# Optimization experiments

Hardware: AMD Instinct MI355X
Metric: run time of the kernel (lower is better)

The kernel has to match this reference:

```python
import jax, jax.numpy as jnp
import numpy as np

T_STEPS = 16
A = 64
B = 64
N = 16          # read_N
C = 3           # channels
H = 1024        # enc_size
IN = N * N * C  # LSTM input size = 768
EPS = 1e-8


def setup_inputs() -> dict:
    key = jax.random.key(0)
    ks = jax.random.split(key, 12)
    s = 0.02
    x = jax.random.normal(ks[0], (1024, C, B, A), dtype=jnp.float32)
    W_att = jax.random.normal(ks[1], (5, H), dtype=jnp.float32) * s
    b_att = jnp.zeros((5,), dtype=jnp.float32)
    W_ih = jax.random.normal(ks[2], (4 * H, IN), dtype=jnp.float32) * s
    W_hh = jax.random.normal(ks[3], (4 * H, H), dtype=jnp.float32) * s
    b_ih = jnp.zeros((4 * H,), dtype=jnp.float32)
    b_hh = jnp.zeros((4 * H,), dtype=jnp.float32)
    W_fc0 = jax.random.normal(ks[4], (H, H), dtype=jnp.float32) * s
    b_fc0 = jnp.zeros((H,), dtype=jnp.float32)
    W_fc = jax.random.normal(ks[5], (10, H), dtype=jnp.float32) * s
    b_fc = jnp.zeros((10,), dtype=jnp.float32)
    return {"x": x, "W_att": W_att, "b_att": b_att, "W_ih": W_ih, "W_hh": W_hh,
            "b_ih": b_ih, "b_hh": b_hh, "W_fc0": W_fc0, "b_fc0": b_fc0,
            "W_fc": W_fc, "b_fc": b_fc}


def _filterbank(gx, gy, sigma2, delta):
    # gx, gy, sigma2, delta: [Bt]
    grid = jnp.arange(N, dtype=jnp.float32)
    mu_x = gx[:, None] + (grid - N / 2 - 0.5) * delta[:, None]   # [Bt, N]
    mu_y = gy[:, None] + (grid - N / 2 - 0.5) * delta[:, None]   # [Bt, N]
    a = jnp.arange(A, dtype=jnp.float32)
    b = jnp.arange(B, dtype=jnp.float32)
    s2 = sigma2[:, None, None]
    Fx = jnp.exp(-(a[None, None, :] - mu_x[:, :, None]) ** 2 / (2 * s2))  # [Bt,N,A]
    Fy = jnp.exp(-(b[None, None, :] - mu_y[:, :, None]) ** 2 / (2 * s2))  # [Bt,N,B]
    Fx = Fx / (Fx.sum(2, keepdims=True) + EPS)
    Fy = Fy / (Fy.sum(2, keepdims=True) + EPS)
    return Fx, Fy


def _forward(x, W_att, b_att, W_ih, W_hh, b_ih, b_hh, W_fc0, b_fc0, W_fc, b_fc):
    Bt = x.shape[0]
    img = x.reshape(Bt, C, B, A)
    h0 = jnp.zeros((Bt, H), dtype=x.dtype)
    c0 = jnp.zeros((Bt, H), dtype=x.dtype)

    def step(carry, _):
        h, c = carry
        p = h @ W_att.T + b_att                      # [Bt, 5]
        gx_, gy_, log_s2, log_d, log_g = (p[:, 0], p[:, 1], p[:, 2], p[:, 3], p[:, 4])
        gx = (A + 1) / 2 * (gx_ + 1)
        gy = (B + 1) / 2 * (gy_ + 1)
        delta = (max(A, B) - 1) / (N - 1) * jnp.exp(log_d)
        sigma2 = jnp.exp(log_s2)
        gamma = jnp.exp(log_g)
        Fx, Fy = _filterbank(gx, gy, sigma2, delta)
        # glimpse[b,c] = Fy @ img[b,c] @ Fx^T -> [Bt, C, N, N]
        glimpse = jnp.einsum('bny,bcya,bxa->bcnx', Fy, img, Fx)
        r = glimpse.reshape(Bt, IN) * gamma[:, None]
        gates = r @ W_ih.T + b_ih + h @ W_hh.T + b_hh
        i_g, f_g, g_g, o_g = jnp.split(gates, 4, axis=1)
        c_new = jax.nn.sigmoid(f_g) * c + jax.nn.sigmoid(i_g) * jnp.tanh(g_g)
        h_new = jax.nn.sigmoid(o_g) * jnp.tanh(c_new)
        return (h_new, c_new), None

    (h, _), _ = jax.lax.scan(step, (h0, c0), None, length=T_STEPS)
    t = jax.nn.relu(h @ W_fc0.T + b_fc0)
    return t @ W_fc.T + b_fc


def reference(x, W_att, b_att, W_ih, W_hh, b_ih, b_hh, W_fc0, b_fc0, W_fc, b_fc):
    return _forward(x, W_att, b_att, W_ih, W_hh, b_ih, b_hh, W_fc0, b_fc0, W_fc, b_fc)
```

## Files before the change

### kernel.cpp

```cpp
#include <hip/hip_runtime.h>

typedef unsigned short u16;
typedef unsigned int u32;
typedef _Float16 f16;
typedef _Float16 half8 __attribute__((ext_vector_type(8)));
typedef _Float16 half4 __attribute__((ext_vector_type(4)));
typedef float f32x4 __attribute__((ext_vector_type(4)));

#define SPLIT_SC 2048.0f
#define SPLIT_INV (1.0f / 2048.0f)

__device__ __forceinline__ float sigf(float x) { return 1.0f / (1.0f + expf(-x)); }

__global__ __launch_bounds__(256) void att_glimpse(
    const f16* __restrict__ h_hi, const f16* __restrict__ h_lo,
    const float* __restrict__ Watt, const float* __restrict__ batt,
    const float* __restrict__ x,
    f16* __restrict__ r_hi, f16* __restrict__ r_lo)
{
    __shared__ float simg[64 * 64];
    __shared__ float sFx[16 * 68];
    __shared__ float sFyT[64 * 20];
    __shared__ float stmp[16 * 68];
    __shared__ float sred[4 * 5];
    __shared__ float spar[8];

    const int b = blockIdx.x, tid = threadIdx.x;
    const int lane = tid & 63, wave = tid >> 6;

    float p[5] = {0.f, 0.f, 0.f, 0.f, 0.f};
    {
        const f16* hh = h_hi + (size_t)b * 1024;
        const f16* hl = h_lo + (size_t)b * 1024;
        for (int k = tid; k < 1024; k += 256) {
            float hv = (float)hh[k] + (float)hl[k] * SPLIT_INV;
#pragma unroll
            for (int j = 0; j < 5; j++) p[j] += hv * Watt[j * 1024 + k];
        }
#pragma unroll
        for (int j = 0; j < 5; j++) {
#pragma unroll
            for (int o = 32; o > 0; o >>= 1) p[j] += __shfl_xor(p[j], o);
        }
        if (lane == 0) {
#pragma unroll
            for (int j = 0; j < 5; j++) sred[wave * 5 + j] = p[j];
        }
    }
    __syncthreads();
    if (tid == 0) {
        float q[5];
#pragma unroll
        for (int j = 0; j < 5; j++)
            q[j] = sred[j] + sred[5 + j] + sred[10 + j] + sred[15 + j] + batt[j];
        float q2 = fminf(fmaxf(q[2], -60.f), 60.f);
        float q3 = fminf(fmaxf(q[3], -60.f), 60.f);
        float q4 = fminf(fmaxf(q[4], -60.f), 60.f);
        spar[0] = 32.5f * (q[0] + 1.0f);
        spar[1] = 32.5f * (q[1] + 1.0f);
        spar[2] = 0.5f * expf(-q2);
        spar[3] = 4.2f * expf(q3);
        spar[4] = expf(q4);
    }
    __syncthreads();
    const float gx = spar[0], gy = spar[1], inv2s2 = spar[2], dl = spar[3],
                gamma = spar[4];

    {
        const float af = (float)lane;
#pragma unroll
        for (int i = 0; i < 4; i++) {
            int n = wave + i * 4;
            float nn = (float)n - 8.5f;
            float mux = gx + nn * dl;
            float ex = af - mux;
            float vx = expf(-ex * ex * inv2s2);
            float sx = vx;
#pragma unroll
            for (int o = 32; o > 0; o >>= 1) sx += __shfl_xor(sx, o);
            sFx[n * 68 + lane] = vx / (sx + 1e-8f);

            float muy = gy + nn * dl;
            float ey = af - muy;
            float vy = expf(-ey * ey * inv2s2);
            float sy = vy;
#pragma unroll
            for (int o = 32; o > 0; o >>= 1) sy += __shfl_xor(sy, o);
            sFyT[lane * 20 + n] = vy / (sy + 1e-8f);
        }
    }

    for (int c = 0; c < 3; c++) {
        __syncthreads();
        {
            const float4* src = (const float4*)(x + (size_t)b * 12288 + c * 4096);
            float4* dst = (float4*)simg;
            for (int i = tid; i < 1024; i += 256) dst[i] = src[i];
        }
        __syncthreads();

        {
            const int n4 = wave, ysub = lane >> 4, a4 = lane & 15;
            f32x4 acc[4];
#pragma unroll
            for (int j = 0; j < 4; j++) acc[j] = (f32x4)(0.f);
            for (int yy = 0; yy < 16; yy++) {
                int y = ysub * 16 + yy;
                float4 im = *(const float4*)(simg + y * 64 + a4 * 4);
                float4 fy = *(const float4*)(sFyT + y * 20 + n4 * 4);
                f32x4 iv = {im.x, im.y, im.z, im.w};
                acc[0] += fy.x * iv;
                acc[1] += fy.y * iv;
                acc[2] += fy.z * iv;
                acc[3] += fy.w * iv;
            }
#pragma unroll
            for (int j = 0; j < 4; j++) {
#pragma unroll
                for (int o = 16; o <= 32; o <<= 1) {
                    acc[j].x += __shfl_xor(acc[j].x, o);
                    acc[j].y += __shfl_xor(acc[j].y, o);
                    acc[j].z += __shfl_xor(acc[j].z, o);
                    acc[j].w += __shfl_xor(acc[j].w, o);
                }
            }
            if (ysub == 0) {
#pragma unroll
                for (int j = 0; j < 4; j++)
                    *(f32x4*)(stmp + (n4 * 4 + j) * 68 + a4 * 4) = acc[j];
            }
        }
        __syncthreads();

        {
            const int n = tid >> 4, xo = tid & 15;
            const float* tp = stmp + n * 68;
            const float* fx = sFx + xo * 68;
            float s = 0.f;
            for (int a = 0; a < 64; a += 4) {
                float4 t4 = *(const float4*)(tp + a);
                float4 x4 = *(const float4*)(fx + a);
                s += t4.x * x4.x + t4.y * x4.y + t4.z * x4.z + t4.w * x4.w;
            }
            float v = s * gamma;
            f16 hi = (f16)v;
            size_t idx = (size_t)b * 768 + c * 256 + tid;
            r_hi[idx] = hi;
            r_lo[idx] = (f16)((v - (float)hi) * SPLIT_SC);
        }
    }
}

__global__ __launch_bounds__(256) void swz_w(
    const float* __restrict__ W1, const float* __restrict__ W2,
    f16* __restrict__ out)
{
    const int kc = blockIdx.x >> 5, bn = blockIdx.x & 31;
    for (int t = threadIdx.x; t < 512; t += 256) {
        int c = t >> 6, lane = t & 63, l15 = lane & 15, lq = lane >> 4;
        int gate = ((c & 1) << 1) + (l15 >> 3);
        int ul   = ((c >> 1) << 3) + (l15 & 7);
        int wrow = gate * 1024 + bn * 32 + ul;
        const float* src;
        if (kc < 24) src = W1 + (size_t)wrow * 768 + kc * 32 + lq * 8;
        else         src = W2 + (size_t)wrow * 1024 + (kc - 24) * 32 + lq * 8;
        float4 g0 = *(const float4*)src;
        float4 g1 = *(const float4*)(src + 4);
        float gv[8] = {g0.x, g0.y, g0.z, g0.w, g1.x, g1.y, g1.z, g1.w};
        half8 hv, lv;
#pragma unroll
        for (int j = 0; j < 8; j++) {
            f16 h = (f16)gv[j];
            hv[j] = h;
            lv[j] = (f16)((gv[j] - (float)h) * SPLIT_SC);
        }
        size_t base = ((size_t)(kc * 32 + bn) * 16 + c * 2) * 512 + (size_t)lane * 8;
        *(half8*)(out + base) = hv;
        *(half8*)(out + base + 512) = lv;
    }
}

#define LDH 40

__global__ __launch_bounds__(256, 2) void gates_lstm(
    const f16* __restrict__ A1h, const f16* __restrict__ A1l,
    const f16* __restrict__ A2h, const f16* __restrict__ A2l,
    const f16* __restrict__ Wswz,
    const float* __restrict__ b1, const float* __restrict__ b2,
    float* __restrict__ cst,
    f16* __restrict__ Hh, f16* __restrict__ Hl)
{
    __shared__ f16 sA[2][2][64 * LDH];
    const int tid = threadIdx.x;
    const int kb = blockIdx.x;
    const int xcd = kb & 7, jb = kb >> 3;
    const int bn = xcd * 4 + (jb & 3);
    const int bm = jb >> 2;
    const int wave = tid >> 6, lane = tid & 63;
    const int cbase = wave * 2;
    const int l15 = lane & 15, lq = lane >> 4;
    const int arow = tid >> 2, acol = (tid & 3) * 8;

    f32x4 ah[4][2], al[4][2];
#pragma unroll
    for (int i = 0; i < 4; i++)
#pragma unroll
        for (int j = 0; j < 2; j++) { ah[i][j] = (f32x4)(0.f); al[i][j] = (f32x4)(0.f); }

    {
        size_t aoff = (size_t)(bm * 64 + arow) * 768 + acol;
        *(uint4*)&sA[0][0][arow * LDH + acol] = *(const uint4*)(A1h + aoff);
        *(uint4*)&sA[0][1][arow * LDH + acol] = *(const uint4*)(A1l + aoff);
    }
    half8 Bc[4];
    {
        const f16* wb = Wswz + (size_t)bn * 16 * 512 + (size_t)lane * 8;
#pragma unroll
        for (int nt = 0; nt < 2; nt++) {
            Bc[nt * 2]     = *(const half8*)(wb + (cbase + nt) * 1024);
            Bc[nt * 2 + 1] = *(const half8*)(wb + (cbase + nt) * 1024 + 512);
        }
    }

#pragma unroll 2
    for (int i = 0; i < 56; ++i) {
        const int cur = i & 1;
        __syncthreads();
        const int kn = (i + 1 < 56) ? i + 1 : 55;
        const f16 *pah, *pal; int astr, ako;
        if (kn < 24) { pah = A1h; pal = A1l; astr = 768;  ako = kn * 32; }
        else         { pah = A2h; pal = A2l; astr = 1024; ako = (kn - 24) * 32; }
        size_t aoff = (size_t)(bm * 64 + arow) * astr + ako + acol;
        uint4 vh = *(const uint4*)(pah + aoff);
        uint4 vl = *(const uint4*)(pal + aoff);
        half8 Bn[4];
        {
            const f16* wb = Wswz + (size_t)(kn * 32 + bn) * 16 * 512 + (size_t)lane * 8;
#pragma unroll
            for (int nt = 0; nt < 2; nt++) {
                Bn[nt * 2]     = *(const half8*)(wb + (cbase + nt) * 1024);
                Bn[nt * 2 + 1] = *(const half8*)(wb + (cbase + nt) * 1024 + 512);
            }
        }
        half8 afh[4], afl[4];
#pragma unroll
        for (int mt = 0; mt < 4; mt++) {
            int ro = (mt * 16 + l15) * LDH + lq * 8;
            afh[mt] = *(const half8*)&sA[cur][0][ro];
            afl[mt] = *(const half8*)&sA[cur][1][ro];
        }
#pragma unroll
        for (int mt = 0; mt < 4; mt++)
#pragma unroll
            for (int nt = 0; nt < 2; nt++) {
                ah[mt][nt] = __builtin_amdgcn_mfma_f32_16x16x32_f16(
                    afh[mt], Bc[nt * 2], ah[mt][nt], 0, 0, 0);
                al[mt][nt] = __builtin_amdgcn_mfma_f32_16x16x32_f16(
                    afh[mt], Bc[nt * 2 + 1], al[mt][nt], 0, 0, 0);
                al[mt][nt] = __builtin_amdgcn_mfma_f32_16x16x32_f16(
                    afl[mt], Bc[nt * 2], al[mt][nt], 0, 0, 0);
            }
        const int nxt = cur ^ 1;
        *(uint4*)&sA[nxt][0][arow * LDH + acol] = vh;
        *(uint4*)&sA[nxt][1][arow * LDH + acol] = vl;
#pragma unroll
        for (int q = 0; q < 4; q++) Bc[q] = Bn[q];
    }

    const int g0 = l15 >> 3;
    const int u = bn * 32 + wave * 8 + (l15 & 7);
    const float bv0 = b1[g0 * 1024 + u] + b2[g0 * 1024 + u];
    const float bv1 = b1[(g0 + 2) * 1024 + u] + b2[(g0 + 2) * 1024 + u];
#pragma unroll
    for (int mt = 0; mt < 4; mt++) {
#pragma unroll
        for (int rg = 0; rg < 4; rg++) {
            int row = bm * 64 + mt * 16 + lq * 4 + rg;
            size_t idx = (size_t)row * 1024 + u;
            float mine0 = ah[mt][0][rg] + al[mt][0][rg] * SPLIT_INV + bv0;
            float mine1 = ah[mt][1][rg] + al[mt][1][rg] * SPLIT_INV + bv1;
            float oth0 = __shfl_xor(mine0, 8);
            float oth1 = __shfl_xor(mine1, 8);
            float gi = (g0 == 0) ? mine0 : oth0;
            float gg = (g0 == 0) ? mine1 : oth1;
            float gf = (g0 == 0) ? oth0 : mine0;
            float go = (g0 == 0) ? oth1 : mine1;
            if (g0 == 0) {
                float cn = sigf(gf) * cst[idx] + sigf(gi) * tanhf(gg);
                float hn = sigf(go) * tanhf(cn);
                cst[idx] = cn;
                f16 hh = (f16)hn;
                Hh[idx] = hh;
                Hl[idx] = (f16)((hn - (float)hh) * SPLIT_SC);
            }
        }
    }
}

__global__ __launch_bounds__(256) void fc0_gemm(
    const f16* __restrict__ Ah, const f16* __restrict__ Al,
    const float* __restrict__ W, const float* __restrict__ bias,
    float* __restrict__ out)
{
    __shared__ f16 sAh[64 * LDH], sAl[64 * LDH];
    __shared__ f16 sBh[64 * LDH], sBl[64 * LDH];
    const int tid = threadIdx.x;
    const int bm = blockIdx.x, bn = blockIdx.y;
    const int wave = tid >> 6, lane = tid & 63;
    const int wm = (wave >> 1) * 32, wn = (wave & 1) * 32;
    const int l15 = lane & 15, lq = lane >> 4;

    f32x4 ach[2][2], acx[2][2];
#pragma unroll
    for (int i = 0; i < 2; i++)
#pragma unroll
        for (int j = 0; j < 2; j++) { ach[i][j] = (f32x4)(0.f); acx[i][j] = (f32x4)(0.f); }

    for (int kc = 0; kc < 1024; kc += 32) {
        {
            int e = tid * 8;
            int row = e >> 5, col = e & 31;
            size_t off = (size_t)(bm * 64 + row) * 1024 + kc + col;
            *(uint4*)&sAh[row * LDH + col] = *(const uint4*)(Ah + off);
            *(uint4*)&sAl[row * LDH + col] = *(const uint4*)(Al + off);
        }
#pragma unroll
        for (int l = 0; l < 2; l++) {
            int e = (l * 256 + tid) * 4;
            int crow = e >> 5, col = e & 31;
            float4 g = *(const float4*)(W + (size_t)(bn * 64 + crow) * 1024 + kc + col);
            f16 h0 = (f16)g.x, h1 = (f16)g.y, h2 = (f16)g.z, h3 = (f16)g.w;
            half4 hv = {h0, h1, h2, h3};
            half4 lv = {(f16)((g.x - (float)h0) * SPLIT_SC),
                        (f16)((g.y - (float)h1) * SPLIT_SC),
                        (f16)((g.z - (float)h2) * SPLIT_SC),
                        (f16)((g.w - (float)h3) * SPLIT_SC)};
            *(half4*)&sBh[crow * LDH + col] = hv;
            *(half4*)&sBl[crow * LDH + col] = lv;
        }
        __syncthreads();
        half8 afh[2], afl[2], bfh[2], bfl[2];
#pragma unroll
        for (int mt = 0; mt < 2; mt++) {
            int ro = (wm + mt * 16 + l15) * LDH + lq * 8;
            afh[mt] = *(const half8*)&sAh[ro];
            afl[mt] = *(const half8*)&sAl[ro];
        }
#pragma unroll
        for (int nt = 0; nt < 2; nt++) {
            int ro = (wn + nt * 16 + l15) * LDH + lq * 8;
            bfh[nt] = *(const half8*)&sBh[ro];
            bfl[nt] = *(const half8*)&sBl[ro];
        }
#pragma unroll
        for (int mt = 0; mt < 2; mt++)
#pragma unroll
            for (int nt = 0; nt < 2; nt++) {
                ach[mt][nt] = __builtin_amdgcn_mfma_f32_16x16x32_f16(
                    afh[mt], bfh[nt], ach[mt][nt], 0, 0, 0);
                acx[mt][nt] = __builtin_amdgcn_mfma_f32_16x16x32_f16(
                    afh[mt], bfl[nt], acx[mt][nt], 0, 0, 0);
                acx[mt][nt] = __builtin_amdgcn_mfma_f32_16x16x32_f16(
                    afl[mt], bfh[nt], acx[mt][nt], 0, 0, 0);
            }
        __syncthreads();
    }

#pragma unroll
    for (int mt = 0; mt < 2; mt++) {
#pragma unroll
        for (int nt = 0; nt < 2; nt++) {
            int col = bn * 64 + wn + nt * 16 + l15;
            float bv = bias[col];
#pragma unroll
            for (int rg = 0; rg < 4; rg++) {
                int row = bm * 64 + wm + mt * 16 + lq * 4 + rg;
                float v = ach[mt][nt][rg] + acx[mt][nt][rg] * SPLIT_INV + bv;
                out[(size_t)row * 1024 + col] = fmaxf(v, 0.f);
            }
        }
    }
}

__global__ __launch_bounds__(64) void fc_out(
    const float* __restrict__ tb, const float* __restrict__ Wfc,
    const float* __restrict__ bfc, float* __restrict__ out)
{
    int b = blockIdx.x, lane = threadIdx.x;
    const float* tv = tb + (size_t)b * 1024;
    float p[10];
#pragma unroll
    for (int j = 0; j < 10; j++) p[j] = 0.f;
    for (int k = lane; k < 1024; k += 64) {
        float t = tv[k];
#pragma unroll
        for (int j = 0; j < 10; j++) p[j] += t * Wfc[j * 1024 + k];
    }
#pragma unroll
    for (int j = 0; j < 10; j++) {
#pragma unroll
        for (int o = 32; o > 0; o >>= 1) p[j] += __shfl_xor(p[j], o);
    }
    if (lane == 0) {
#pragma unroll
        for (int j = 0; j < 10; j++) out[b * 10 + j] = p[j] + bfc[j];
    }
}

extern "C" void kernel_launch(void* const* d_in, const int* in_sizes, int n_in,
                              void* d_out, int out_size, void* d_ws, size_t ws_size,
                              hipStream_t stream)
{
    const float* x     = (const float*)d_in[0];
    const float* W_att = (const float*)d_in[1];
    const float* b_att = (const float*)d_in[2];
    const float* W_ih  = (const float*)d_in[3];
    const float* W_hh  = (const float*)d_in[4];
    const float* b_ih  = (const float*)d_in[5];
    const float* b_hh  = (const float*)d_in[6];
    const float* W_fc0 = (const float*)d_in[7];
    const float* b_fc0 = (const float*)d_in[8];
    const float* W_fc  = (const float*)d_in[9];
    const float* b_fc  = (const float*)d_in[10];
    float* out = (float*)d_out;

    char* ws = (char*)d_ws;
    f16*   Wswz   = (f16*)ws;    ws += (size_t)56 * 32 * 16 * 512 * 2;
    float* c_f32  = (float*)ws;  ws += (size_t)1024 * 1024 * 4;
    f16*   h_hi0  = (f16*)ws;    ws += (size_t)1024 * 1024 * 2;
    f16*   h_hi1  = (f16*)ws;    ws += (size_t)1024 * 1024 * 2;
    f16*   h_lo0  = (f16*)ws;    ws += (size_t)1024 * 1024 * 2;
    f16*   h_lo1  = (f16*)ws;    ws += (size_t)1024 * 1024 * 2;
    f16*   r_hi   = (f16*)ws;    ws += (size_t)1024 * 768 * 2;
    f16*   r_lo   = (f16*)ws;    ws += (size_t)1024 * 768 * 2;
    float* t_f32  = c_f32;
    f16* h_hi[2] = {h_hi0, h_hi1};
    f16* h_lo[2] = {h_lo0, h_lo1};

    hipMemsetAsync(c_f32, 0, (size_t)1024 * 1024 * 4, stream);
    hipMemsetAsync(h_hi0, 0, (size_t)1024 * 1024 * 2, stream);
    hipMemsetAsync(h_lo0, 0, (size_t)1024 * 1024 * 2, stream);

    swz_w<<<56 * 32, 256, 0, stream>>>(W_ih, W_hh, Wswz);

    for (int t = 0; t < 16; t++) {
        int rb = t & 1, wb = 1 - rb;
        att_glimpse<<<1024, 256, 0, stream>>>(
            h_hi[rb], h_lo[rb], W_att, b_att, x, r_hi, r_lo);
        gates_lstm<<<512, 256, 0, stream>>>(
            r_hi, r_lo, h_hi[rb], h_lo[rb], Wswz, b_ih, b_hh,
            c_f32, h_hi[wb], h_lo[wb]);
    }
    fc0_gemm<<<dim3(16, 16), 256, 0, stream>>>(
        h_hi[0], h_lo[0], W_fc0, b_fc0, t_f32);
    fc_out<<<1024, 64, 0, stream>>>(t_f32, W_fc, b_fc, out);
}
```

Before: 1.401 ms.

## Double K-step per barrier in LSTM gates GEMM; read glimpse image directly from global

The gates GEMM now handles 64 K-columns per iteration, split into two 32-wide sub-steps, so it runs 28 iterations instead of 56. This halves the number of barriers and prefetch rounds, at the cost of a larger LDS tile and twice as many weight registers held in flight. The attention-glimpse kernel no longer stages each image channel in shared memory. It reads float4s straight from global memory with the y-loop fully unrolled, removing a barrier and an LDS copy but relying on cache for the repeated reads.

```diff
diff --git a/kernel.cpp b/kernel.cpp
--- a/kernel.cpp
+++ b/kernel.cpp
@@ -18,7 +18,6 @@
     const float* __restrict__ x,
     f16* __restrict__ r_hi, f16* __restrict__ r_lo)
 {
-    __shared__ float simg[64 * 64];
     __shared__ float sFx[16 * 68];
     __shared__ float sFyT[64 * 20];
     __shared__ float stmp[16 * 68];
@@ -92,21 +91,17 @@
 
     for (int c = 0; c < 3; c++) {
         __syncthreads();
-        {
-            const float4* src = (const float4*)(x + (size_t)b * 12288 + c * 4096);
-            float4* dst = (float4*)simg;
-            for (int i = tid; i < 1024; i += 256) dst[i] = src[i];
-        }
-        __syncthreads();
 
         {
             const int n4 = wave, ysub = lane >> 4, a4 = lane & 15;
+            const float* xg = x + (size_t)b * 12288 + c * 4096;
             f32x4 acc[4];
 #pragma unroll
             for (int j = 0; j < 4; j++) acc[j] = (f32x4)(0.f);
+#pragma unroll
             for (int yy = 0; yy < 16; yy++) {
                 int y = ysub * 16 + yy;
-                float4 im = *(const float4*)(simg + y * 64 + a4 * 4);
+                float4 im = *(const float4*)(xg + y * 64 + a4 * 4);
                 float4 fy = *(const float4*)(sFyT + y * 20 + n4 * 4);
                 f32x4 iv = {im.x, im.y, im.z, im.w};
                 acc[0] += fy.x * iv;
@@ -180,7 +175,7 @@
     }
 }
 
-#define LDH 40
+#define LDH2 72
 
 __global__ __launch_bounds__(256, 2) void gates_lstm(
     const f16* __restrict__ A1h, const f16* __restrict__ A1l,
@@ -190,7 +185,7 @@
     float* __restrict__ cst,
     f16* __restrict__ Hh, f16* __restrict__ Hl)
 {
-    __shared__ f16 sA[2][2][64 * LDH];
+    __shared__ f16 sA[2][2][64 * LDH2];
     const int tid = threadIdx.x;
     const int kb = blockIdx.x;
     const int xcd = kb & 7, jb = kb >> 3;
@@ -199,7 +194,7 @@
     const int wave = tid >> 6, lane = tid & 63;
     const int cbase = wave * 2;
     const int l15 = lane & 15, lq = lane >> 4;
-    const int arow = tid >> 2, acol = (tid & 3) * 8;
+    const int arow = tid >> 3, acol = (tid & 7) * 8;
 
     f32x4 ah[4][2], al[4][2];
 #pragma unroll
@@ -208,63 +203,77 @@
         for (int j = 0; j < 2; j++) { ah[i][j] = (f32x4)(0.f); al[i][j] = (f32x4)(0.f); }
 
     {
-        size_t aoff = (size_t)(bm * 64 + arow) * 768 + acol;
-        *(uint4*)&sA[0][0][arow * LDH + acol] = *(const uint4*)(A1h + aoff);
-        *(uint4*)&sA[0][1][arow * LDH + acol] = *(const uint4*)(A1l + aoff);
-    }
-    half8 Bc[4];
-    {
-        const f16* wb = Wswz + (size_t)bn * 16 * 512 + (size_t)lane * 8;
+        size_t a0 = (size_t)(bm * 64 + arow) * 768 + acol;
+        size_t a1 = (size_t)(bm * 64 + arow + 32) * 768 + acol;
+        *(uint4*)&sA[0][0][arow * LDH2 + acol]        = *(const uint4*)(A1h + a0);
+        *(uint4*)&sA[0][0][(arow + 32) * LDH2 + acol] = *(const uint4*)(A1h + a1);
+        *(uint4*)&sA[0][1][arow * LDH2 + acol]        = *(const uint4*)(A1l + a0);
+        *(uint4*)&sA[0][1][(arow + 32) * LDH2 + acol] = *(const uint4*)(A1l + a1);
+    }
+    half8 Bc[8];
+#pragma unroll
+    for (int sub = 0; sub < 2; sub++) {
+        const f16* wb = Wswz + (size_t)(sub * 32 + bn) * 16 * 512 + (size_t)lane * 8;
 #pragma unroll
         for (int nt = 0; nt < 2; nt++) {
-            Bc[nt * 2]     = *(const half8*)(wb + (cbase + nt) * 1024);
-            Bc[nt * 2 + 1] = *(const half8*)(wb + (cbase + nt) * 1024 + 512);
+            Bc[sub * 4 + nt * 2]     = *(const half8*)(wb + (cbase + nt) * 1024);
+            Bc[sub * 4 + nt * 2 + 1] = *(const half8*)(wb + (cbase + nt) * 1024 + 512);
         }
     }
 
 #pragma unroll 2
-    for (int i = 0; i < 56; ++i) {
+    for (int i = 0; i < 28; ++i) {
         const int cur = i & 1;
         __syncthreads();
-        const int kn = (i + 1 < 56) ? i + 1 : 55;
+        const int kn = (i + 1 < 28) ? i + 1 : 27;
         const f16 *pah, *pal; int astr, ako;
-        if (kn < 24) { pah = A1h; pal = A1l; astr = 768;  ako = kn * 32; }
-        else         { pah = A2h; pal = A2l; astr = 1024; ako = (kn - 24) * 32; }
-        size_t aoff = (size_t)(bm * 64 + arow) * astr + ako + acol;
-        uint4 vh = *(const uint4*)(pah + aoff);
-        uint4 vl = *(const uint4*)(pal + aoff);
-        half8 Bn[4];
-        {
-            const f16* wb = Wswz + (size_t)(kn * 32 + bn) * 16 * 512 + (size_t)lane * 8;
+        if (kn < 12) { pah = A1h; pal = A1l; astr = 768;  ako = kn * 64; }
+        else         { pah = A2h; pal = A2l; astr = 1024; ako = (kn - 12) * 64; }
+        size_t a0 = (size_t)(bm * 64 + arow) * astr + ako + acol;
+        size_t a1 = (size_t)(bm * 64 + arow + 32) * astr + ako + acol;
+        uint4 vh0 = *(const uint4*)(pah + a0);
+        uint4 vh1 = *(const uint4*)(pah + a1);
+        uint4 vl0 = *(const uint4*)(pal + a0);
+        uint4 vl1 = *(const uint4*)(pal + a1);
+        half8 Bn[8];
+#pragma unroll
+        for (int sub = 0; sub < 2; sub++) {
+            const f16* wb = Wswz + (size_t)((kn * 2 + sub) * 32 + bn) * 16 * 512
+                          + (size_t)lane * 8;
 #pragma unroll
             for (int nt = 0; nt < 2; nt++) {
-                Bn[nt * 2]     = *(const half8*)(wb + (cbase + nt) * 1024);
-                Bn[nt * 2 + 1] = *(const half8*)(wb + (cbase + nt) * 1024 + 512);
-            }
-        }
-        half8 afh[4], afl[4];
-#pragma unroll
-        for (int mt = 0; mt < 4; mt++) {
-            int ro = (mt * 16 + l15) * LDH + lq * 8;
-            afh[mt] = *(const half8*)&sA[cur][0][ro];
-            afl[mt] = *(const half8*)&sA[cur][1][ro];
-        }
-#pragma unroll
-        for (int mt = 0; mt < 4; mt++)
-#pragma unroll
-            for (int nt = 0; nt < 2; nt++) {
-                ah[mt][nt] = __builtin_amdgcn_mfma_f32_16x16x32_f16(
-                    afh[mt], Bc[nt * 2], ah[mt][nt], 0, 0, 0);
-                al[mt][nt] = __builtin_amdgcn_mfma_f32_16x16x32_f16(
-                    afh[mt], Bc[nt * 2 + 1], al[mt][nt], 0, 0, 0);
-                al[mt][nt] = __builtin_amdgcn_mfma_f32_16x16x32_f16(
-                    afl[mt], Bc[nt * 2], al[mt][nt], 0, 0, 0);
-            }
+                Bn[sub * 4 + nt * 2]     = *(const half8*)(wb + (cbase + nt) * 1024);
+                Bn[sub * 4 + nt * 2 + 1] = *(const half8*)(wb + (cbase + nt) * 1024 + 512);
+            }
+        }
+#pragma unroll
+        for (int sub = 0; sub < 2; sub++) {
+            half8 afh[4], afl[4];
+#pragma unroll
+            for (int mt = 0; mt < 4; mt++) {
+                int ro = (mt * 16 + l15) * LDH2 + sub * 32 + lq * 8;
+                afh[mt] = *(const half8*)&sA[cur][0][ro];
+                afl[mt] = *(const half8*)&sA[cur][1][ro];
+            }
+#pragma unroll
+            for (int mt = 0; mt < 4; mt++)
+#pragma unroll
+                for (int nt = 0; nt < 2; nt++) {
+                    ah[mt][nt] = __builtin_amdgcn_mfma_f32_16x16x32_f16(
+                        afh[mt], Bc[sub * 4 + nt * 2], ah[mt][nt], 0, 0, 0);
+                    al[mt][nt] = __builtin_amdgcn_mfma_f32_16x16x32_f16(
+                        afh[mt], Bc[sub * 4 + nt * 2 + 1], al[mt][nt], 0, 0, 0);
+                    al[mt][nt] = __builtin_amdgcn_mfma_f32_16x16x32_f16(
+                        afl[mt], Bc[sub * 4 + nt * 2], al[mt][nt], 0, 0, 0);
+                }
+        }
         const int nxt = cur ^ 1;
-        *(uint4*)&sA[nxt][0][arow * LDH + acol] = vh;
-        *(uint4*)&sA[nxt][1][arow * LDH + acol] = vl;
-#pragma unroll
-        for (int q = 0; q < 4; q++) Bc[q] = Bn[q];
+        *(uint4*)&sA[nxt][0][arow * LDH2 + acol]        = vh0;
+        *(uint4*)&sA[nxt][0][(arow + 32) * LDH2 + acol] = vh1;
+        *(uint4*)&sA[nxt][1][arow * LDH2 + acol]        = vl0;
+        *(uint4*)&sA[nxt][1][(arow + 32) * LDH2 + acol] = vl1;
+#pragma unroll
+        for (int q = 0; q < 8; q++) Bc[q] = Bn[q];
     }
 
     const int g0 = l15 >> 3;
@@ -297,6 +306,8 @@
     }
 }
 
+#define LDH 40
+
 __global__ __launch_bounds__(256) void fc0_gemm(
     const f16* __restrict__ Ah, const f16* __restrict__ Al,
     const float* __restrict__ W, const float* __restrict__ bias,
```

Result: faster. 1.321 ms (-5.7%).
